# Performance work log

Measured on AMD Instinct MI355X. Metric: run time of the kernel, lower is better.

The kernel has to match this reference:

```python
import jax, jax.numpy as jnp
import numpy as np

B, T, N, H, DK = 4, 16, 256, 8, 64

def setup_inputs() -> dict:
    key = jax.random.key(0)
    k1, k2, k3 = jax.random.split(key, 3)
    queries = jax.random.normal(k1, (B, T, N, H, DK), dtype=jnp.float32)
    keys = jax.random.normal(k2, (B, T, N, H, DK), dtype=jnp.float32)
    values = jax.random.normal(k3, (B, T, N, H, DK), dtype=jnp.float32)
    attention_mask = jnp.zeros((B, T, 1, N, N), dtype=bool)  # unused: mask_flag=False
    return {"queries": queries, "keys": keys, "values": values, "attention_mask": attention_mask}

def reference(queries, keys, values, attention_mask):
    # queries: B T N H d_k; keys/values: B T S H d_k/d_v
    d_k = queries.shape[-1]
    scale = 1.0 / jnp.sqrt(jnp.asarray(d_k, queries.dtype))
    # scores: B T H N S
    scores = jnp.einsum('btnhe,btshe->bthns', queries, keys)
    # mask_flag=False -> no masking; dropout is identity in eval mode
    A = jax.nn.softmax(scale * scores, axis=-1)
    V = jnp.einsum('bthns,btshd->btnhd', A, values)
    return V
```

## Files before the change

### kernel.cpp

```cpp
#include <hip/hip_runtime.h>


typedef short short8 __attribute__((ext_vector_type(8)));
typedef float floatx4 __attribute__((ext_vector_type(4)));

__device__ __forceinline__ unsigned cvt_pk(float lo, float hi) {
  unsigned r;
  asm("v_cvt_pk_bf16_f32 %0, %1, %2" : "=v"(r) : "v"(lo), "v"(hi));
  return r;
}

constexpr int KSTR = 72;
constexpr int VSTR = 264;

__global__ __launch_bounds__(512, 4) void attn_kernel(
    const float* __restrict__ Q, const float* __restrict__ K,
    const float* __restrict__ V, float* __restrict__ O) {
  __shared__ __align__(16) short Klds[256 * KSTR];
  __shared__ __align__(16) short Vt[64 * VSTR];

  const int inst = blockIdx.x;
  const int h    = inst & 7;
  const int bt   = inst >> 3;
  const int base = bt * (256 * 512) + h * 64;
  const int tid  = threadIdx.x;

  {
    const float* Kb = K + base;
    #pragma unroll
    for (int i = 0; i < 8; ++i) {
      int idx = i * 512 + tid;
      int s = idx >> 4, c4 = idx & 15;
      float4 v = *reinterpret_cast<const float4*>(Kb + s * 512 + c4 * 4);
      uint2 w;
      w.x = cvt_pk(v.x, v.y);
      w.y = cvt_pk(v.z, v.w);
      *reinterpret_cast<uint2*>(&Klds[s * KSTR + c4 * 4]) = w;
    }
  }
  {
    const float* Vb = V + base;
    unsigned* Vt32 = reinterpret_cast<unsigned*>(Vt);
    #pragma unroll
    for (int i = 0; i < 4; ++i) {
      int idx = i * 512 + tid;
      int sp = idx >> 4, c4 = idx & 15;
      int s = sp * 2;
      float4 v0 = *reinterpret_cast<const float4*>(Vb + s * 512 + c4 * 4);
      float4 v1 = *reinterpret_cast<const float4*>(Vb + (s + 1) * 512 + c4 * 4);
      #pragma unroll
      for (int k = 0; k < 4; ++k) {
        Vt32[(c4 * 4 + k) * (VSTR / 2) + sp] = cvt_pk((&v0.x)[k], (&v1.x)[k]);
      }
    }
  }

  const int wave = tid >> 6;
  const int lane = tid & 63;
  const int c    = lane & 15;
  const int g    = lane >> 4;

  const float SCQ = 0.125f * 1.4426950408889634f;
  short8 qf[2][2];
  #pragma unroll
  for (int p = 0; p < 2; ++p) {
    #pragma unroll
    for (int ks2 = 0; ks2 < 2; ++ks2) {
      const float* qp =
          Q + base + (p * 128 + wave * 16 + c) * 512 + ks2 * 32 + g * 8;
      float4 a = *reinterpret_cast<const float4*>(qp);
      float4 b = *reinterpret_cast<const float4*>(qp + 4);
      union { unsigned u[4]; short8 s; } t;
      t.u[0] = cvt_pk(a.x * SCQ, a.y * SCQ);
      t.u[1] = cvt_pk(a.z * SCQ, a.w * SCQ);
      t.u[2] = cvt_pk(b.x * SCQ, b.y * SCQ);
      t.u[3] = cvt_pk(b.z * SCQ, b.w * SCQ);
      qf[p][ks2] = t.s;
    }
  }
  __syncthreads();

  floatx4 ao[2][4];
  #pragma unroll
  for (int p = 0; p < 2; ++p)
    #pragma unroll
    for (int dt = 0; dt < 4; ++dt) ao[p][dt] = floatx4{0.f, 0.f, 0.f, 0.f};
  float ps[2][4] = {{0.f, 0.f, 0.f, 0.f}, {0.f, 0.f, 0.f, 0.f}};

  #pragma unroll
  for (int ks = 0; ks < 8; ++ks) {
    unsigned pk2[2][2][2];
    #pragma unroll
    for (int tt = 0; tt < 2; ++tt) {
      const int t = 2 * ks + tt;
      short8 kf0 = *reinterpret_cast<const short8*>(
          &Klds[(t * 16 + c) * KSTR + g * 8]);
      short8 kf1 = *reinterpret_cast<const short8*>(
          &Klds[(t * 16 + c) * KSTR + 32 + g * 8]);
      #pragma unroll
      for (int p = 0; p < 2; ++p) {
        floatx4 acc = {0.f, 0.f, 0.f, 0.f};
        acc = __builtin_amdgcn_mfma_f32_16x16x32_bf16(kf0, qf[p][0], acc, 0, 0, 0);
        acc = __builtin_amdgcn_mfma_f32_16x16x32_bf16(kf1, qf[p][1], acc, 0, 0, 0);
        float e0 = exp2f(acc[0]);
        float e1 = exp2f(acc[1]);
        float e2 = exp2f(acc[2]);
        float e3 = exp2f(acc[3]);
        ps[p][0] += e0; ps[p][1] += e1; ps[p][2] += e2; ps[p][3] += e3;
        pk2[p][tt][0] = cvt_pk(e0, e1);
        pk2[p][tt][1] = cvt_pk(e2, e3);
      }
    }

    union { unsigned u[4]; short8 s; } pa[2];
    #pragma unroll
    for (int p = 0; p < 2; ++p) {
      #pragma unroll
      for (int m = 0; m < 2; ++m) {
        unsigned x = pk2[p][0][m], y = pk2[p][1][m];
        asm("v_permlane32_swap_b32 %0, %1" : "+v"(x), "+v"(y));
        asm("v_permlane16_swap_b32 %0, %1" : "+v"(x), "+v"(y));
        pa[p].u[m]     = x;
        pa[p].u[2 + m] = y;
      }
    }

    #pragma unroll
    for (int dt = 0; dt < 4; ++dt) {
      short8 vf = *reinterpret_cast<const short8*>(
          &Vt[(dt * 16 + c) * VSTR + ks * 32 + g * 8]);
      ao[0][dt] = __builtin_amdgcn_mfma_f32_16x16x32_bf16(pa[0].s, vf, ao[0][dt], 0, 0, 0);
      ao[1][dt] = __builtin_amdgcn_mfma_f32_16x16x32_bf16(pa[1].s, vf, ao[1][dt], 0, 0, 0);
    }
  }

  #pragma unroll
  for (int p = 0; p < 2; ++p) {
    const int n0 = p * 128 + wave * 16;
    float sum = (ps[p][0] + ps[p][1]) + (ps[p][2] + ps[p][3]);
    sum += __shfl_xor(sum, 16);
    sum += __shfl_xor(sum, 32);
    const float rcp = __builtin_amdgcn_rcpf(sum);
    float rcpv[4];
    #pragma unroll
    for (int r = 0; r < 4; ++r) rcpv[r] = __shfl(rcp, 4 * g + r);
    #pragma unroll
    for (int dt = 0; dt < 4; ++dt)
      #pragma unroll
      for (int r = 0; r < 4; ++r)
        O[base + (n0 + 4 * g + r) * 512 + dt * 16 + c] = ao[p][dt][r] * rcpv[r];
  }
}

extern "C" void kernel_launch(void* const* d_in, const int* in_sizes, int n_in,
                              void* d_out, int out_size, void* d_ws, size_t ws_size,
                              hipStream_t stream) {
  const float* Q = (const float*)d_in[0];
  const float* K = (const float*)d_in[1];
  const float* V = (const float*)d_in[2];
  float* O = (float*)d_out;
  attn_kernel<<<dim3(512), dim3(512), 0, stream>>>(Q, K, V, O);
}
```

Measured before the change: 30.77 us.

## Swizzle V-transpose LDS, stagger and prefetch K reads, split QK MFMA chains

Replaces the padded V-transpose layout with an XOR-swizzled word layout to reduce LDS bank conflicts on both the transpose writes and the fragment reads. Each wave now starts its key loop at a different offset so waves do not hit the same LDS rows at once. K fragments for the next tile are prefetched while the current one is used. The two dependent QK MFMAs become independent ones whose results are added. Output stores become nontemporal. Together these aim to cut LDS stalls and MFMA dependency latency, at the cost of more registers and more complex indexing.

```diff
diff --git a/kernel.cpp b/kernel.cpp
--- a/kernel.cpp
+++ b/kernel.cpp
@@ -10,14 +10,14 @@
   return r;
 }
 
-constexpr int KSTR = 72;
-constexpr int VSTR = 264;
+constexpr int KSTR  = 72;
+constexpr int VSTRW = 132;
 
 __global__ __launch_bounds__(512, 4) void attn_kernel(
     const float* __restrict__ Q, const float* __restrict__ K,
     const float* __restrict__ V, float* __restrict__ O) {
   __shared__ __align__(16) short Klds[256 * KSTR];
-  __shared__ __align__(16) short Vt[64 * VSTR];
+  __shared__ __align__(16) unsigned Vt32[64 * VSTRW];
 
   const int inst = blockIdx.x;
   const int h    = inst & 7;
@@ -40,17 +40,17 @@
   }
   {
     const float* Vb = V + base;
-    unsigned* Vt32 = reinterpret_cast<unsigned*>(Vt);
     #pragma unroll
     for (int i = 0; i < 4; ++i) {
       int idx = i * 512 + tid;
       int sp = idx >> 4, c4 = idx & 15;
       int s = sp * 2;
+      int spw = sp ^ ((c4 & 7) << 2);
       float4 v0 = *reinterpret_cast<const float4*>(Vb + s * 512 + c4 * 4);
       float4 v1 = *reinterpret_cast<const float4*>(Vb + (s + 1) * 512 + c4 * 4);
       #pragma unroll
       for (int k = 0; k < 4; ++k) {
-        Vt32[(c4 * 4 + k) * (VSTR / 2) + sp] = cvt_pk((&v0.x)[k], (&v1.x)[k]);
+        Vt32[(c4 * 4 + k) * VSTRW + spw] = cvt_pk((&v0.x)[k], (&v1.x)[k]);
       }
     }
   }
@@ -80,6 +80,13 @@
   }
   __syncthreads();
 
+#define KREAD(t, half) \
+  (*reinterpret_cast<const short8*>(&Klds[((t) * 16 + c) * KSTR + (half) * 32 + g * 8]))
+#define VREAD(dt, ks) \
+  (*reinterpret_cast<const short8*>(reinterpret_cast<const short*>( \
+      &Vt32[((dt) * 16 + c) * VSTRW + \
+            (((ks) * 16 + 4 * g) ^ (16 * ((dt) & 1) + (c & 12)))])))
+
   floatx4 ao[2][4];
   #pragma unroll
   for (int p = 0; p < 2; ++p)
@@ -87,28 +94,56 @@
     for (int dt = 0; dt < 4; ++dt) ao[p][dt] = floatx4{0.f, 0.f, 0.f, 0.f};
   float ps[2][4] = {{0.f, 0.f, 0.f, 0.f}, {0.f, 0.f, 0.f, 0.f}};
 
-  #pragma unroll
-  for (int ks = 0; ks < 8; ++ks) {
+  const int ksW = wave & 7;
+  short8 kfa = KREAD(2 * ksW, 0);
+  short8 kfb = KREAD(2 * ksW, 1);
+
+  #pragma unroll
+  for (int kk = 0; kk < 8; ++kk) {
+    const int ks  = (kk + ksW) & 7;
+    const int ksn = (ks + 1) & 7;
     unsigned pk2[2][2][2];
-    #pragma unroll
-    for (int tt = 0; tt < 2; ++tt) {
-      const int t = 2 * ks + tt;
-      short8 kf0 = *reinterpret_cast<const short8*>(
-          &Klds[(t * 16 + c) * KSTR + g * 8]);
-      short8 kf1 = *reinterpret_cast<const short8*>(
-          &Klds[(t * 16 + c) * KSTR + 32 + g * 8]);
+
+    {
+      short8 ka = kfa, kb = kfb;
+      kfa = KREAD(2 * ks + 1, 0);
+      kfb = KREAD(2 * ks + 1, 1);
       #pragma unroll
       for (int p = 0; p < 2; ++p) {
-        floatx4 acc = {0.f, 0.f, 0.f, 0.f};
-        acc = __builtin_amdgcn_mfma_f32_16x16x32_bf16(kf0, qf[p][0], acc, 0, 0, 0);
-        acc = __builtin_amdgcn_mfma_f32_16x16x32_bf16(kf1, qf[p][1], acc, 0, 0, 0);
-        float e0 = exp2f(acc[0]);
-        float e1 = exp2f(acc[1]);
-        float e2 = exp2f(acc[2]);
-        float e3 = exp2f(acc[3]);
+        floatx4 z = {0.f, 0.f, 0.f, 0.f};
+        floatx4 a0 = __builtin_amdgcn_mfma_f32_16x16x32_bf16(ka, qf[p][0], z, 0, 0, 0);
+        floatx4 a1 = __builtin_amdgcn_mfma_f32_16x16x32_bf16(kb, qf[p][1], z, 0, 0, 0);
+        float e0 = exp2f(a0[0] + a1[0]);
+        float e1 = exp2f(a0[1] + a1[1]);
+        float e2 = exp2f(a0[2] + a1[2]);
+        float e3 = exp2f(a0[3] + a1[3]);
         ps[p][0] += e0; ps[p][1] += e1; ps[p][2] += e2; ps[p][3] += e3;
-        pk2[p][tt][0] = cvt_pk(e0, e1);
-        pk2[p][tt][1] = cvt_pk(e2, e3);
+        pk2[p][0][0] = cvt_pk(e0, e1);
+        pk2[p][0][1] = cvt_pk(e2, e3);
+      }
+    }
+
+    short8 vf0 = VREAD(0, ks);
+    short8 vf1 = VREAD(1, ks);
+    short8 vf2 = VREAD(2, ks);
+    short8 vf3 = VREAD(3, ks);
+
+    {
+      short8 ka = kfa, kb = kfb;
+      kfa = KREAD(2 * ksn, 0);
+      kfb = KREAD(2 * ksn, 1);
+      #pragma unroll
+      for (int p = 0; p < 2; ++p) {
+        floatx4 z = {0.f, 0.f, 0.f, 0.f};
+        floatx4 a0 = __builtin_amdgcn_mfma_f32_16x16x32_bf16(ka, qf[p][0], z, 0, 0, 0);
+        floatx4 a1 = __builtin_amdgcn_mfma_f32_16x16x32_bf16(kb, qf[p][1], z, 0, 0, 0);
+        float e0 = exp2f(a0[0] + a1[0]);
+        float e1 = exp2f(a0[1] + a1[1]);
+        float e2 = exp2f(a0[2] + a1[2]);
+        float e3 = exp2f(a0[3] + a1[3]);
+        ps[p][0] += e0; ps[p][1] += e1; ps[p][2] += e2; ps[p][3] += e3;
+        pk2[p][1][0] = cvt_pk(e0, e1);
+        pk2[p][1][1] = cvt_pk(e2, e3);
       }
     }
 
@@ -125,13 +160,14 @@
       }
     }
 
-    #pragma unroll
-    for (int dt = 0; dt < 4; ++dt) {
-      short8 vf = *reinterpret_cast<const short8*>(
-          &Vt[(dt * 16 + c) * VSTR + ks * 32 + g * 8]);
-      ao[0][dt] = __builtin_amdgcn_mfma_f32_16x16x32_bf16(pa[0].s, vf, ao[0][dt], 0, 0, 0);
-      ao[1][dt] = __builtin_amdgcn_mfma_f32_16x16x32_bf16(pa[1].s, vf, ao[1][dt], 0, 0, 0);
-    }
+    ao[0][0] = __builtin_amdgcn_mfma_f32_16x16x32_bf16(pa[0].s, vf0, ao[0][0], 0, 0, 0);
+    ao[1][0] = __builtin_amdgcn_mfma_f32_16x16x32_bf16(pa[1].s, vf0, ao[1][0], 0, 0, 0);
+    ao[0][1] = __builtin_amdgcn_mfma_f32_16x16x32_bf16(pa[0].s, vf1, ao[0][1], 0, 0, 0);
+    ao[1][1] = __builtin_amdgcn_mfma_f32_16x16x32_bf16(pa[1].s, vf1, ao[1][1], 0, 0, 0);
+    ao[0][2] = __builtin_amdgcn_mfma_f32_16x16x32_bf16(pa[0].s, vf2, ao[0][2], 0, 0, 0);
+    ao[1][2] = __builtin_amdgcn_mfma_f32_16x16x32_bf16(pa[1].s, vf2, ao[1][2], 0, 0, 0);
+    ao[0][3] = __builtin_amdgcn_mfma_f32_16x16x32_bf16(pa[0].s, vf3, ao[0][3], 0, 0, 0);
+    ao[1][3] = __builtin_amdgcn_mfma_f32_16x16x32_bf16(pa[1].s, vf3, ao[1][3], 0, 0, 0);
   }
 
   #pragma unroll
@@ -148,8 +184,12 @@
     for (int dt = 0; dt < 4; ++dt)
       #pragma unroll
       for (int r = 0; r < 4; ++r)
-        O[base + (n0 + 4 * g + r) * 512 + dt * 16 + c] = ao[p][dt][r] * rcpv[r];
-  }
+        __builtin_nontemporal_store(
+            ao[p][dt][r] * rcpv[r],
+            &O[base + (n0 + 4 * g + r) * 512 + dt * 16 + c]);
+  }
+#undef KREAD
+#undef VREAD
 }
 
 extern "C" void kernel_launch(void* const* d_in, const int* in_sizes, int n_in,
```

After: 29.99 us. -2.5%, faster.

## Double-buffer K/V tiles in LDS and prefetch next chunk during compute

Applied to the files above, without the earlier changes.

Replaces the full up-front load of all 256 K/V rows into shared memory with a 4-step loop over 64-row chunks. Each step issues global loads for the next chunk, computes on the current buffer, then converts and stores the next chunk into the other buffer. The intent is to overlap global load latency with MFMA work and cut LDS footprint, which could raise occupancy. The V transpose layout now uses an XOR swizzle instead of padding, and the two QK MFMAs use independent accumulators that are summed afterwards. It adds a barrier per chunk.

```diff
diff --git a/kernel.cpp b/kernel.cpp
--- a/kernel.cpp
+++ b/kernel.cpp
@@ -10,14 +10,14 @@
   return r;
 }
 
-constexpr int KSTR = 72;
-constexpr int VSTR = 264;
+constexpr int KSTR  = 72;
+constexpr int VSTRW = 36;
 
 __global__ __launch_bounds__(512, 4) void attn_kernel(
     const float* __restrict__ Q, const float* __restrict__ K,
     const float* __restrict__ V, float* __restrict__ O) {
-  __shared__ __align__(16) short Klds[256 * KSTR];
-  __shared__ __align__(16) short Vt[64 * VSTR];
+  __shared__ __align__(16) short    Klds[2][64 * KSTR];
+  __shared__ __align__(16) unsigned Vt32[2][64 * VSTRW];
 
   const int inst = blockIdx.x;
   const int h    = inst & 7;
@@ -25,40 +25,15 @@
   const int base = bt * (256 * 512) + h * 64;
   const int tid  = threadIdx.x;
 
-  {
-    const float* Kb = K + base;
-    #pragma unroll
-    for (int i = 0; i < 8; ++i) {
-      int idx = i * 512 + tid;
-      int s = idx >> 4, c4 = idx & 15;
-      float4 v = *reinterpret_cast<const float4*>(Kb + s * 512 + c4 * 4);
-      uint2 w;
-      w.x = cvt_pk(v.x, v.y);
-      w.y = cvt_pk(v.z, v.w);
-      *reinterpret_cast<uint2*>(&Klds[s * KSTR + c4 * 4]) = w;
-    }
-  }
-  {
-    const float* Vb = V + base;
-    unsigned* Vt32 = reinterpret_cast<unsigned*>(Vt);
-    #pragma unroll
-    for (int i = 0; i < 4; ++i) {
-      int idx = i * 512 + tid;
-      int sp = idx >> 4, c4 = idx & 15;
-      int s = sp * 2;
-      float4 v0 = *reinterpret_cast<const float4*>(Vb + s * 512 + c4 * 4);
-      float4 v1 = *reinterpret_cast<const float4*>(Vb + (s + 1) * 512 + c4 * 4);
-      #pragma unroll
-      for (int k = 0; k < 4; ++k) {
-        Vt32[(c4 * 4 + k) * (VSTR / 2) + sp] = cvt_pk((&v0.x)[k], (&v1.x)[k]);
-      }
-    }
-  }
-
   const int wave = tid >> 6;
   const int lane = tid & 63;
   const int c    = lane & 15;
   const int g    = lane >> 4;
+  const int c4   = tid & 15;
+  const int sQ   = tid >> 4;
+
+  const float* Kb = K + base;
+  const float* Vb = V + base;
 
   const float SCQ = 0.125f * 1.4426950408889634f;
   short8 qf[2][2];
@@ -78,7 +53,33 @@
       qf[p][ks2] = t.s;
     }
   }
+
+  #pragma unroll
+  for (int i = 0; i < 2; ++i) {
+    int sr = i * 32 + sQ;
+    float4 v = *reinterpret_cast<const float4*>(Kb + sr * 512 + c4 * 4);
+    uint2 w;
+    w.x = cvt_pk(v.x, v.y);
+    w.y = cvt_pk(v.z, v.w);
+    *reinterpret_cast<uint2*>(&Klds[0][sr * KSTR + c4 * 4]) = w;
+  }
+  {
+    int spw = sQ ^ ((c4 & 7) << 2);
+    float4 v0 = *reinterpret_cast<const float4*>(Vb + (2 * sQ) * 512 + c4 * 4);
+    float4 v1 = *reinterpret_cast<const float4*>(Vb + (2 * sQ + 1) * 512 + c4 * 4);
+    #pragma unroll
+    for (int k = 0; k < 4; ++k)
+      Vt32[0][(c4 * 4 + k) * VSTRW + spw] = cvt_pk((&v0.x)[k], (&v1.x)[k]);
+  }
   __syncthreads();
+
+#define KREAD(buf, ts, half)                                       \
+  (*reinterpret_cast<const short8*>(                               \
+      &Klds[buf][((ts) * 16 + c) * KSTR + (half) * 32 + g * 8]))
+#define VREAD(buf, dt, ksc)                                        \
+  (*reinterpret_cast<const short8*>(reinterpret_cast<const short*>(\
+      &Vt32[buf][((dt) * 16 + c) * VSTRW +                         \
+                 (((ksc) * 16 + 4 * g) ^ (16 * ((dt) & 1) + (c & 12)))])))
 
   floatx4 ao[2][4];
   #pragma unroll
@@ -88,59 +89,93 @@
   float ps[2][4] = {{0.f, 0.f, 0.f, 0.f}, {0.f, 0.f, 0.f, 0.f}};
 
   #pragma unroll
-  for (int ks = 0; ks < 8; ++ks) {
-    unsigned pk2[2][2][2];
-    #pragma unroll
-    for (int tt = 0; tt < 2; ++tt) {
-      const int t = 2 * ks + tt;
-      short8 kf0 = *reinterpret_cast<const short8*>(
-          &Klds[(t * 16 + c) * KSTR + g * 8]);
-      short8 kf1 = *reinterpret_cast<const short8*>(
-          &Klds[(t * 16 + c) * KSTR + 32 + g * 8]);
+  for (int t = 0; t < 4; ++t) {
+    const int cur = t & 1, nxt = cur ^ 1;
+
+    float4 kv0, kv1, vv0, vv1;
+    if (t < 3) {
+      kv0 = *reinterpret_cast<const float4*>(
+          Kb + ((t + 1) * 64 + sQ) * 512 + c4 * 4);
+      kv1 = *reinterpret_cast<const float4*>(
+          Kb + ((t + 1) * 64 + 32 + sQ) * 512 + c4 * 4);
+      vv0 = *reinterpret_cast<const float4*>(
+          Vb + ((t + 1) * 64 + 2 * sQ) * 512 + c4 * 4);
+      vv1 = *reinterpret_cast<const float4*>(
+          Vb + ((t + 1) * 64 + 2 * sQ + 1) * 512 + c4 * 4);
+    }
+
+    unsigned pk[2][4][2];
+    #pragma unroll
+    for (int ts = 0; ts < 4; ++ts) {
+      short8 kf0 = KREAD(cur, ts, 0);
+      short8 kf1 = KREAD(cur, ts, 1);
       #pragma unroll
       for (int p = 0; p < 2; ++p) {
-        floatx4 acc = {0.f, 0.f, 0.f, 0.f};
-        acc = __builtin_amdgcn_mfma_f32_16x16x32_bf16(kf0, qf[p][0], acc, 0, 0, 0);
-        acc = __builtin_amdgcn_mfma_f32_16x16x32_bf16(kf1, qf[p][1], acc, 0, 0, 0);
-        float e0 = exp2f(acc[0]);
-        float e1 = exp2f(acc[1]);
-        float e2 = exp2f(acc[2]);
-        float e3 = exp2f(acc[3]);
+        floatx4 z = {0.f, 0.f, 0.f, 0.f};
+        floatx4 a0 = __builtin_amdgcn_mfma_f32_16x16x32_bf16(kf0, qf[p][0], z, 0, 0, 0);
+        floatx4 a1 = __builtin_amdgcn_mfma_f32_16x16x32_bf16(kf1, qf[p][1], z, 0, 0, 0);
+        float e0 = exp2f(a0[0] + a1[0]);
+        float e1 = exp2f(a0[1] + a1[1]);
+        float e2 = exp2f(a0[2] + a1[2]);
+        float e3 = exp2f(a0[3] + a1[3]);
         ps[p][0] += e0; ps[p][1] += e1; ps[p][2] += e2; ps[p][3] += e3;
-        pk2[p][tt][0] = cvt_pk(e0, e1);
-        pk2[p][tt][1] = cvt_pk(e2, e3);
+        pk[p][ts][0] = cvt_pk(e0, e1);
+        pk[p][ts][1] = cvt_pk(e2, e3);
       }
     }
 
-    union { unsigned u[4]; short8 s; } pa[2];
-    #pragma unroll
-    for (int p = 0; p < 2; ++p) {
-      #pragma unroll
-      for (int m = 0; m < 2; ++m) {
-        unsigned x = pk2[p][0][m], y = pk2[p][1][m];
-        asm("v_permlane32_swap_b32 %0, %1" : "+v"(x), "+v"(y));
-        asm("v_permlane16_swap_b32 %0, %1" : "+v"(x), "+v"(y));
-        pa[p].u[m]     = x;
-        pa[p].u[2 + m] = y;
+    #pragma unroll
+    for (int ksc = 0; ksc < 2; ++ksc) {
+      union { unsigned u[4]; short8 s; } pa[2];
+      #pragma unroll
+      for (int p = 0; p < 2; ++p) {
+        #pragma unroll
+        for (int m = 0; m < 2; ++m) {
+          unsigned x = pk[p][2 * ksc][m], y = pk[p][2 * ksc + 1][m];
+          asm("v_permlane32_swap_b32 %0, %1" : "+v"(x), "+v"(y));
+          asm("v_permlane16_swap_b32 %0, %1" : "+v"(x), "+v"(y));
+          pa[p].u[m]     = x;
+          pa[p].u[2 + m] = y;
+        }
       }
-    }
-
-    #pragma unroll
-    for (int dt = 0; dt < 4; ++dt) {
-      short8 vf = *reinterpret_cast<const short8*>(
-          &Vt[(dt * 16 + c) * VSTR + ks * 32 + g * 8]);
-      ao[0][dt] = __builtin_amdgcn_mfma_f32_16x16x32_bf16(pa[0].s, vf, ao[0][dt], 0, 0, 0);
-      ao[1][dt] = __builtin_amdgcn_mfma_f32_16x16x32_bf16(pa[1].s, vf, ao[1][dt], 0, 0, 0);
-    }
+      short8 vf0 = VREAD(cur, 0, ksc);
+      short8 vf1 = VREAD(cur, 1, ksc);
+      short8 vf2 = VREAD(cur, 2, ksc);
+      short8 vf3 = VREAD(cur, 3, ksc);
+      ao[0][0] = __builtin_amdgcn_mfma_f32_16x16x32_bf16(pa[0].s, vf0, ao[0][0], 0, 0, 0);
+      ao[1][0] = __builtin_amdgcn_mfma_f32_16x16x32_bf16(pa[1].s, vf0, ao[1][0], 0, 0, 0);
+      ao[0][1] = __builtin_amdgcn_mfma_f32_16x16x32_bf16(pa[0].s, vf1, ao[0][1], 0, 0, 0);
+      ao[1][1] = __builtin_amdgcn_mfma_f32_16x16x32_bf16(pa[1].s, vf1, ao[1][1], 0, 0, 0);
+      ao[0][2] = __builtin_amdgcn_mfma_f32_16x16x32_bf16(pa[0].s, vf2, ao[0][2], 0, 0, 0);
+      ao[1][2] = __builtin_amdgcn_mfma_f32_16x16x32_bf16(pa[1].s, vf2, ao[1][2], 0, 0, 0);
+      ao[0][3] = __builtin_amdgcn_mfma_f32_16x16x32_bf16(pa[0].s, vf3, ao[0][3], 0, 0, 0);
+      ao[1][3] = __builtin_amdgcn_mfma_f32_16x16x32_bf16(pa[1].s, vf3, ao[1][3], 0, 0, 0);
+    }
+
+    if (t < 3) {
+      #pragma unroll
+      for (int i = 0; i < 2; ++i) {
+        float4 v = i ? kv1 : kv0;
+        uint2 w;
+        w.x = cvt_pk(v.x, v.y);
+        w.y = cvt_pk(v.z, v.w);
+        *reinterpret_cast<uint2*>(&Klds[nxt][(i * 32 + sQ) * KSTR + c4 * 4]) = w;
+      }
+      int spw = sQ ^ ((c4 & 7) << 2);
+      #pragma unroll
+      for (int k = 0; k < 4; ++k)
+        Vt32[nxt][(c4 * 4 + k) * VSTRW + spw] = cvt_pk((&vv0.x)[k], (&vv1.x)[k]);
+    }
+    __syncthreads();
   }
 
   #pragma unroll
   for (int p = 0; p < 2; ++p) {
     const int n0 = p * 128 + wave * 16;
-    float sum = (ps[p][0] + ps[p][1]) + (ps[p][2] + ps[p][3]);
-    sum += __shfl_xor(sum, 16);
-    sum += __shfl_xor(sum, 32);
-    const float rcp = __builtin_amdgcn_rcpf(sum);
+    float s4 = (ps[p][0] + ps[p][1]) + (ps[p][2] + ps[p][3]);
+    s4 += __shfl_xor(s4, 16);
+    s4 += __shfl_xor(s4, 32);
+    const float rcp = __builtin_amdgcn_rcpf(s4);
     float rcpv[4];
     #pragma unroll
     for (int r = 0; r < 4; ++r) rcpv[r] = __shfl(rcp, 4 * g + r);
@@ -150,6 +185,8 @@
       for (int r = 0; r < 4; ++r)
         O[base + (n0 + 4 * g + r) * 512 + dt * 16 + c] = ao[p][dt][r] * rcpv[r];
   }
+#undef KREAD
+#undef VREAD
 }
 
 extern "C" void kernel_launch(void* const* d_in, const int* in_sizes, int n_in,
```

Measured after the change: 53.62 us. 1.74x slower.

## Switch attention MFMAs to 32x32x16 tiles with swizzled transposed V in LDS

Applied to the files above, without the earlier changes.

Replaces the 16x16x32 bf16 MFMA tiling with 32x32x16 MFMAs, so each wave owns 32 query rows and processes 32 keys per iteration. The P-fragment shuffle now needs only permlane32 swaps. V is stored transposed as 32-bit words with an XOR swizzle to avoid LDS bank conflicts. The goal is fewer instructions and fewer LDS fragment loads per FLOP. The cost is larger accumulators and more registers, so launch bounds drop to 2 blocks per SIMD.

```diff
diff --git a/kernel.cpp b/kernel.cpp
--- a/kernel.cpp
+++ b/kernel.cpp
@@ -2,7 +2,7 @@
 
 
 typedef short short8 __attribute__((ext_vector_type(8)));
-typedef float floatx4 __attribute__((ext_vector_type(4)));
+typedef float floatx16 __attribute__((ext_vector_type(16)));
 
 __device__ __forceinline__ unsigned cvt_pk(float lo, float hi) {
   unsigned r;
@@ -10,145 +10,150 @@
   return r;
 }
 
-constexpr int KSTR = 72;
-constexpr int VSTR = 264;
+constexpr int KSTR  = 72;
+constexpr int VSTRW = 132;
 
-__global__ __launch_bounds__(512, 4) void attn_kernel(
+__global__ __launch_bounds__(512, 2) void attn_kernel(
     const float* __restrict__ Q, const float* __restrict__ K,
     const float* __restrict__ V, float* __restrict__ O) {
-  __shared__ __align__(16) short Klds[256 * KSTR];
-  __shared__ __align__(16) short Vt[64 * VSTR];
+  __shared__ __align__(16) short    Klds[256 * KSTR];
+  __shared__ __align__(16) unsigned Vt32[64 * VSTRW];
 
   const int inst = blockIdx.x;
-  const int h    = inst & 7;
+  const int h8   = inst & 7;
   const int bt   = inst >> 3;
-  const int base = bt * (256 * 512) + h * 64;
+  const int base = bt * (256 * 512) + h8 * 64;
   const int tid  = threadIdx.x;
+
+  const int wave = tid >> 6;
+  const int lane = tid & 63;
+  const int r31  = lane & 31;
+  const int h    = lane >> 5;
+  const int c4   = tid & 15;
+  const int sQ   = tid >> 4;
 
   {
     const float* Kb = K + base;
     #pragma unroll
     for (int i = 0; i < 8; ++i) {
       int idx = i * 512 + tid;
-      int s = idx >> 4, c4 = idx & 15;
-      float4 v = *reinterpret_cast<const float4*>(Kb + s * 512 + c4 * 4);
+      int s = idx >> 4, cc = idx & 15;
+      float4 v = *reinterpret_cast<const float4*>(Kb + s * 512 + cc * 4);
       uint2 w;
       w.x = cvt_pk(v.x, v.y);
       w.y = cvt_pk(v.z, v.w);
-      *reinterpret_cast<uint2*>(&Klds[s * KSTR + c4 * 4]) = w;
+      *reinterpret_cast<uint2*>(&Klds[s * KSTR + cc * 4]) = w;
     }
   }
   {
     const float* Vb = V + base;
-    unsigned* Vt32 = reinterpret_cast<unsigned*>(Vt);
     #pragma unroll
     for (int i = 0; i < 4; ++i) {
       int idx = i * 512 + tid;
-      int sp = idx >> 4, c4 = idx & 15;
+      int sp = idx >> 4, cc = idx & 15;
       int s = sp * 2;
-      float4 v0 = *reinterpret_cast<const float4*>(Vb + s * 512 + c4 * 4);
-      float4 v1 = *reinterpret_cast<const float4*>(Vb + (s + 1) * 512 + c4 * 4);
+      int spw = sp ^ ((cc & 7) << 2);
+      float4 v0 = *reinterpret_cast<const float4*>(Vb + s * 512 + cc * 4);
+      float4 v1 = *reinterpret_cast<const float4*>(Vb + (s + 1) * 512 + cc * 4);
       #pragma unroll
-      for (int k = 0; k < 4; ++k) {
-        Vt32[(c4 * 4 + k) * (VSTR / 2) + sp] = cvt_pk((&v0.x)[k], (&v1.x)[k]);
-      }
+      for (int k = 0; k < 4; ++k)
+        Vt32[(cc * 4 + k) * VSTRW + spw] = cvt_pk((&v0.x)[k], (&v1.x)[k]);
     }
   }
 
-  const int wave = tid >> 6;
-  const int lane = tid & 63;
-  const int c    = lane & 15;
-  const int g    = lane >> 4;
-
   const float SCQ = 0.125f * 1.4426950408889634f;
-  short8 qf[2][2];
+  const int nq = wave * 32 + r31;
+  short8 qf[4];
   #pragma unroll
-  for (int p = 0; p < 2; ++p) {
-    #pragma unroll
-    for (int ks2 = 0; ks2 < 2; ++ks2) {
-      const float* qp =
-          Q + base + (p * 128 + wave * 16 + c) * 512 + ks2 * 32 + g * 8;
-      float4 a = *reinterpret_cast<const float4*>(qp);
-      float4 b = *reinterpret_cast<const float4*>(qp + 4);
-      union { unsigned u[4]; short8 s; } t;
-      t.u[0] = cvt_pk(a.x * SCQ, a.y * SCQ);
-      t.u[1] = cvt_pk(a.z * SCQ, a.w * SCQ);
-      t.u[2] = cvt_pk(b.x * SCQ, b.y * SCQ);
-      t.u[3] = cvt_pk(b.z * SCQ, b.w * SCQ);
-      qf[p][ks2] = t.s;
-    }
+  for (int kc = 0; kc < 4; ++kc) {
+    const float* qp = Q + base + nq * 512 + 16 * kc + 8 * h;
+    float4 a = *reinterpret_cast<const float4*>(qp);
+    float4 b = *reinterpret_cast<const float4*>(qp + 4);
+    union { unsigned u[4]; short8 s; } t;
+    t.u[0] = cvt_pk(a.x * SCQ, a.y * SCQ);
+    t.u[1] = cvt_pk(a.z * SCQ, a.w * SCQ);
+    t.u[2] = cvt_pk(b.x * SCQ, b.y * SCQ);
+    t.u[3] = cvt_pk(b.z * SCQ, b.w * SCQ);
+    qf[kc] = t.s;
   }
   __syncthreads();
 
-  floatx4 ao[2][4];
-  #pragma unroll
-  for (int p = 0; p < 2; ++p)
-    #pragma unroll
-    for (int dt = 0; dt < 4; ++dt) ao[p][dt] = floatx4{0.f, 0.f, 0.f, 0.f};
-  float ps[2][4] = {{0.f, 0.f, 0.f, 0.f}, {0.f, 0.f, 0.f, 0.f}};
+  const int swzr = ((r31 >> 2) & 7) << 2;
+
+  floatx16 ao0 = {}, ao1 = {};
+  float ps[4] = {0.f, 0.f, 0.f, 0.f};
 
   #pragma unroll
-  for (int ks = 0; ks < 8; ++ks) {
-    unsigned pk2[2][2][2];
+  for (int it = 0; it < 8; ++it) {
+    floatx16 sc = {};
     #pragma unroll
-    for (int tt = 0; tt < 2; ++tt) {
-      const int t = 2 * ks + tt;
-      short8 kf0 = *reinterpret_cast<const short8*>(
-          &Klds[(t * 16 + c) * KSTR + g * 8]);
-      short8 kf1 = *reinterpret_cast<const short8*>(
-          &Klds[(t * 16 + c) * KSTR + 32 + g * 8]);
-      #pragma unroll
-      for (int p = 0; p < 2; ++p) {
-        floatx4 acc = {0.f, 0.f, 0.f, 0.f};
-        acc = __builtin_amdgcn_mfma_f32_16x16x32_bf16(kf0, qf[p][0], acc, 0, 0, 0);
-        acc = __builtin_amdgcn_mfma_f32_16x16x32_bf16(kf1, qf[p][1], acc, 0, 0, 0);
-        float e0 = exp2f(acc[0]);
-        float e1 = exp2f(acc[1]);
-        float e2 = exp2f(acc[2]);
-        float e3 = exp2f(acc[3]);
-        ps[p][0] += e0; ps[p][1] += e1; ps[p][2] += e2; ps[p][3] += e3;
-        pk2[p][tt][0] = cvt_pk(e0, e1);
-        pk2[p][tt][1] = cvt_pk(e2, e3);
-      }
+    for (int kc = 0; kc < 4; ++kc) {
+      short8 kf = *reinterpret_cast<const short8*>(
+          &Klds[(32 * it + r31) * KSTR + 16 * kc + 8 * h]);
+      sc = __builtin_amdgcn_mfma_f32_32x32x16_bf16(kf, qf[kc], sc, 0, 0, 0);
     }
 
-    union { unsigned u[4]; short8 s; } pa[2];
+    unsigned pk[8];
     #pragma unroll
-    for (int p = 0; p < 2; ++p) {
-      #pragma unroll
-      for (int m = 0; m < 2; ++m) {
-        unsigned x = pk2[p][0][m], y = pk2[p][1][m];
-        asm("v_permlane32_swap_b32 %0, %1" : "+v"(x), "+v"(y));
-        asm("v_permlane16_swap_b32 %0, %1" : "+v"(x), "+v"(y));
-        pa[p].u[m]     = x;
-        pa[p].u[2 + m] = y;
-      }
+    for (int q = 0; q < 4; ++q) {
+      float e0 = exp2f(sc[4 * q + 0]);
+      float e1 = exp2f(sc[4 * q + 1]);
+      float e2 = exp2f(sc[4 * q + 2]);
+      float e3 = exp2f(sc[4 * q + 3]);
+      ps[q] += (e0 + e1) + (e2 + e3);
+      pk[2 * q]     = cvt_pk(e0, e1);
+      pk[2 * q + 1] = cvt_pk(e2, e3);
     }
 
-    #pragma unroll
-    for (int dt = 0; dt < 4; ++dt) {
-      short8 vf = *reinterpret_cast<const short8*>(
-          &Vt[(dt * 16 + c) * VSTR + ks * 32 + g * 8]);
-      ao[0][dt] = __builtin_amdgcn_mfma_f32_16x16x32_bf16(pa[0].s, vf, ao[0][dt], 0, 0, 0);
-      ao[1][dt] = __builtin_amdgcn_mfma_f32_16x16x32_bf16(pa[1].s, vf, ao[1][dt], 0, 0, 0);
+    union { unsigned u[4]; short8 s; } pa0, pa1;
+    {
+      unsigned x, y;
+      x = pk[0]; y = pk[2];
+      asm("v_permlane32_swap_b32 %0, %1" : "+v"(x), "+v"(y));
+      pa0.u[0] = x; pa0.u[2] = y;
+      x = pk[1]; y = pk[3];
+      asm("v_permlane32_swap_b32 %0, %1" : "+v"(x), "+v"(y));
+      pa0.u[1] = x; pa0.u[3] = y;
+      x = pk[4]; y = pk[6];
+      asm("v_permlane32_swap_b32 %0, %1" : "+v"(x), "+v"(y));
+      pa1.u[0] = x; pa1.u[2] = y;
+      x = pk[5]; y = pk[7];
+      asm("v_permlane32_swap_b32 %0, %1" : "+v"(x), "+v"(y));
+      pa1.u[1] = x; pa1.u[3] = y;
+    }
+
+    {
+      const unsigned* vrow0 = &Vt32[(r31) * VSTRW];
+      const unsigned* vrow1 = &Vt32[(32 + r31) * VSTRW];
+      short8 vf00 = *reinterpret_cast<const short8*>(
+          vrow0 + ((16 * it + 4 * h) ^ swzr));
+      short8 vf01 = *reinterpret_cast<const short8*>(
+          vrow0 + ((16 * it + 8 + 4 * h) ^ swzr));
+      short8 vf10 = *reinterpret_cast<const short8*>(
+          vrow1 + ((16 * it + 4 * h) ^ swzr));
+      short8 vf11 = *reinterpret_cast<const short8*>(
+          vrow1 + ((16 * it + 8 + 4 * h) ^ swzr));
+      ao0 = __builtin_amdgcn_mfma_f32_32x32x16_bf16(pa0.s, vf00, ao0, 0, 0, 0);
+      ao0 = __builtin_amdgcn_mfma_f32_32x32x16_bf16(pa1.s, vf01, ao0, 0, 0, 0);
+      ao1 = __builtin_amdgcn_mfma_f32_32x32x16_bf16(pa0.s, vf10, ao1, 0, 0, 0);
+      ao1 = __builtin_amdgcn_mfma_f32_32x32x16_bf16(pa1.s, vf11, ao1, 0, 0, 0);
     }
   }
 
+  float pstot = (ps[0] + ps[1]) + (ps[2] + ps[3]);
+  pstot += __shfl_xor(pstot, 32);
+  const float rcp = __builtin_amdgcn_rcpf(pstot);
+
+  float rcpv[16];
   #pragma unroll
-  for (int p = 0; p < 2; ++p) {
-    const int n0 = p * 128 + wave * 16;
-    float sum = (ps[p][0] + ps[p][1]) + (ps[p][2] + ps[p][3]);
-    sum += __shfl_xor(sum, 16);
-    sum += __shfl_xor(sum, 32);
-    const float rcp = __builtin_amdgcn_rcpf(sum);
-    float rcpv[4];
-    #pragma unroll
-    for (int r = 0; r < 4; ++r) rcpv[r] = __shfl(rcp, 4 * g + r);
-    #pragma unroll
-    for (int dt = 0; dt < 4; ++dt)
-      #pragma unroll
-      for (int r = 0; r < 4; ++r)
-        O[base + (n0 + 4 * g + r) * 512 + dt * 16 + c] = ao[p][dt][r] * rcpv[r];
+  for (int reg = 0; reg < 16; ++reg)
+    rcpv[reg] = __shfl(rcp, (reg & 3) + 8 * (reg >> 2) + 4 * h);
+
+  #pragma unroll
+  for (int reg = 0; reg < 16; ++reg) {
+    int n = wave * 32 + (reg & 3) + 8 * (reg >> 2) + 4 * h;
+    O[base + n * 512 + r31]      = ao0[reg] * rcpv[reg];
+    O[base + n * 512 + 32 + r31] = ao1[reg] * rcpv[reg];
   }
 }
 
```

Result: slower. 33.80 us (+9.9%).
